# Performance work log

Measured on AMD Instinct MI355X. Metric: run time of the kernel, lower is better.

Reference implementation:

```python
import jax, jax.numpy as jnp
import numpy as np

B, C, H, W = 16, 64, 128, 128
C8 = C // 8


def setup_inputs() -> dict:
    key = jax.random.key(0)
    ks = jax.random.split(key, 8)
    s = 0.05
    return {
        "x": jax.random.normal(ks[0], (B, C, H, W), dtype=jnp.float32),
        "Wq": jax.random.normal(ks[1], (C8, C), dtype=jnp.float32) * s,
        "bq": jax.random.normal(ks[2], (C8,), dtype=jnp.float32) * s,
        "Wk": jax.random.normal(ks[3], (C8, C), dtype=jnp.float32) * s,
        "bk": jax.random.normal(ks[4], (C8,), dtype=jnp.float32) * s,
        "Wv": jax.random.normal(ks[5], (C, C), dtype=jnp.float32) * s,
        "bv": jax.random.normal(ks[6], (C,), dtype=jnp.float32) * s,
        "gamma": jnp.zeros((1,), dtype=jnp.float32),
    }


def _criss_cross(x, Wq, bq, Wk, bk, Wv, bv, gamma):
    # 1x1 convs == channel-mixing matmuls
    q = jnp.einsum("bchw,oc->bohw", x, Wq) + bq[None, :, None, None]  # [B,C8,H,W]
    k = jnp.einsum("bchw,oc->bohw", x, Wk) + bk[None, :, None, None]  # [B,C8,H,W]
    v = jnp.einsum("bchw,oc->bohw", x, Wv) + bv[None, :, None, None]  # [B,C,H,W]

    h = x.shape[2]
    # column (H-axis) attention scores; diagonal masked to -inf
    energy_H = jnp.einsum("bchw,bciw->bhwi", q, k)  # [B,H,W,H]
    diag = jnp.eye(h, dtype=bool)[None, :, None, :]  # mask where query row == key row
    energy_H = jnp.where(diag, -jnp.inf, energy_H)
    # row (W-axis) attention scores
    energy_W = jnp.einsum("bchw,bchj->bhwj", q, k)  # [B,H,W,W]

    # joint softmax over concatenated H+W axis
    att = jax.nn.softmax(jnp.concatenate([energy_H, energy_W], axis=3), axis=3)
    att_H = att[:, :, :, :h]    # [B,H,W,H]
    att_W = att[:, :, :, h:]    # [B,H,W,W]

    out_H = jnp.einsum("bhwi,bciw->bchw", att_H, v)
    out_W = jnp.einsum("bhwj,bchj->bchw", att_W, v)
    return gamma[0] * (out_H + out_W) + x


def reference(x, Wq, bq, Wk, bk, Wv, bv, gamma):
    return _criss_cross(x, Wq, bq, Wk, bk, Wv, bv, gamma)
```

## Files before the change

### kernel.cpp

```cpp
#include <hip/hip_runtime.h>

#define HW 128
#define CC 64
#define C8V 8
#define NB 16
#define LOG2E 1.44269504088896f

typedef _Float16 h1;
typedef _Float16 h2 __attribute__((ext_vector_type(2)));
typedef _Float16 half8 __attribute__((ext_vector_type(8)));
typedef float float16v __attribute__((ext_vector_type(16)));
typedef uint uv4 __attribute__((ext_vector_type(4)));

__device__ __forceinline__ uint packh2(float a, float b) {
#if __has_builtin(__builtin_amdgcn_cvt_pkrtz)
  return __builtin_bit_cast(uint, __builtin_amdgcn_cvt_pkrtz(a, b));
#else
  h2 v; v[0] = (h1)a; v[1] = (h1)b; return __builtin_bit_cast(uint, v);
#endif
}
__device__ __forceinline__ ushort f2h(float a) { h1 v = (h1)a; return __builtin_bit_cast(ushort, v); }
__device__ __forceinline__ float  h2f(ushort a) { return (float)__builtin_bit_cast(h1, a); }

__device__ __forceinline__ float fexp2(float x) {
#if __has_builtin(__builtin_amdgcn_exp2f)
  return __builtin_amdgcn_exp2f(x);
#else
  return exp2f(x);
#endif
}

__device__ __forceinline__ float16v mfma16(uv4 a, uv4 b, float16v c) {
  return __builtin_amdgcn_mfma_f32_32x32x16_f16(
      __builtin_bit_cast(half8, a), __builtin_bit_cast(half8, b), c, 0, 0, 0);
}

__global__ __launch_bounds__(256) void k_prep(
    const float* __restrict__ Wq, const float* __restrict__ bq,
    const float* __restrict__ Wk, const float* __restrict__ bk,
    const float* __restrict__ Wv, const float* __restrict__ bv,
    ushort* __restrict__ W_frag, float* __restrict__ bias_f)
{
  int idx = blockIdx.x * 256 + threadIdx.x;
  if (idx < 6144) {
    int g = idx >> 3, e = idx & 7;
    int kshi = g / 96, o = g % 96;
    int ks = kshi >> 1, hi = kshi & 1;
    int c = 8 * hi + 16 * ks + e;
    float val = (o < 8)  ? Wq[o * 64 + c] * LOG2E
              : (o < 16) ? Wk[(o - 8) * 64 + c]
              : (o < 80) ? Wv[(o - 16) * 64 + c] : 0.f;
    W_frag[idx] = f2h(val);
  }
  if (blockIdx.x == 0 && threadIdx.x < 96) {
    int t = threadIdx.x;
    bias_f[t] = (t < 8) ? bq[t] * LOG2E : (t < 16) ? bk[t - 8] : (t < 80) ? bv[t - 16] : 0.f;
  }
}

__global__ __launch_bounds__(256) void k_proj(
    const float* __restrict__ x, const ushort* __restrict__ W_frag,
    const float* __restrict__ bias_f,
    ushort* __restrict__ q, ushort* __restrict__ k,
    ushort* __restrict__ qT, ushort* __restrict__ kT,
    ushort* __restrict__ v)
{
  alignas(16) __shared__ ushort smem[10496];
  __shared__ float bias_l[96];
  ushort* o_l  = smem;
  ushort* qk_l = smem + 8192;

  int t = threadIdx.x;
  int lane = t & 63, wv = t >> 6, hi = lane >> 5;
  int b = blockIdx.x >> 7, r = blockIdx.x & 127;
  if (t < 96) bias_l[t] = bias_f[t];

  int w = 32 * wv + (lane & 31);
  const float* xw = x + (size_t)(b * CC) * (HW * HW) + (size_t)r * HW + w;
  const size_t PL = (size_t)HW * HW;

  float16v acc0 = {}, acc1 = {}, acc2 = {};
  #pragma unroll
  for (int ks = 0; ks < 4; ++ks) {
    int c0 = 8 * hi + 16 * ks;
    uint bx[4];
    #pragma unroll
    for (int e2 = 0; e2 < 4; ++e2) {
      float f0 = xw[(size_t)(c0 + 2 * e2) * PL];
      float f1 = xw[(size_t)(c0 + 2 * e2 + 1) * PL];
      bx[e2] = packh2(f0, f1);
    }
    uv4 Bx = {bx[0], bx[1], bx[2], bx[3]};
    const ushort* wf = W_frag + (size_t)(ks * 2 + hi) * 96 * 8;
    uv4 a0 = *(const uv4*)(wf + (lane & 31) * 8);
    uv4 a1 = *(const uv4*)(wf + ((lane & 31) + 32) * 8);
    uv4 a2 = *(const uv4*)(wf + ((lane & 31) + 64) * 8);
    acc0 = mfma16(a0, Bx, acc0);
    acc1 = mfma16(a1, Bx, acc1);
    acc2 = mfma16(a2, Bx, acc2);
  }
  __syncthreads();

  #pragma unroll
  for (int reg = 0; reg < 16; ++reg) {
    int orow = (reg & 3) + 8 * (reg >> 2) + 4 * hi;
    float v0 = acc0[reg] + bias_l[orow];
    if (orow < 16) qk_l[w * 18 + orow] = f2h(v0);
    else           o_l[(orow - 16) * 128 + w] = f2h(v0);
    o_l[(orow + 16) * 128 + w] = f2h(acc1[reg] + bias_l[orow + 32]);
    if (orow < 16)
      o_l[(orow + 48) * 128 + w] = f2h(acc2[reg] + bias_l[orow + 64]);
  }
  __syncthreads();

  {
    int pix = t & 127, isk = t >> 7;
    const ushort* src = &qk_l[pix * 18 + isk * 8];
    uint d0 = *(const uint*)(src + 0);
    uint d1 = *(const uint*)(src + 2);
    uint d2 = *(const uint*)(src + 4);
    uint d3 = *(const uint*)(src + 6);
    uv4 val = {d0, d1, d2, d3};
    ushort* dstn = (isk ? k : q)  + ((size_t)(b * HW + r) * HW + pix) * 8;
    ushort* dstt = (isk ? kT : qT) + ((size_t)(b * HW + pix) * HW + r) * 8;
    *(uv4*)dstn = val;
    *(uv4*)dstt = val;
  }
  ushort* vb = v + (size_t)(b * CC) * PL + (size_t)r * HW;
  #pragma unroll
  for (int i = 0; i < 4; ++i) {
    int idx = t + 256 * i; int o_ = idx >> 4, w8 = idx & 15;
    *(uv4*)(vb + (size_t)o_ * PL + w8 * 8) = *(const uv4*)&o_l[o_ * 128 + w8 * 8];
  }
}

__global__ __launch_bounds__(256) void k_transpose_v(const ushort* __restrict__ v,
                                                     ushort* __restrict__ vT)
{
  __shared__ ushort tl[128 * 130];
  int t = threadIdx.x;
  size_t base = (size_t)blockIdx.x * (HW * HW);
  const uint* ip = (const uint*)(v + base);
  uint* op = (uint*)(vT + base);
  int c2 = t & 63;
  int r0 = t >> 6;
  for (int it = 0; it < 32; ++it) {
    int r = it * 4 + r0;
    uint val = ip[r * 64 + c2];
    *(uint*)&tl[r * 130 + c2 * 2] = val;
  }
  __syncthreads();
  for (int it = 0; it < 32; ++it) {
    int wcol = it * 4 + r0;
    int hh = c2 * 2;
    uint lo = tl[hh * 130 + wcol];
    uint hi = tl[(hh + 1) * 130 + wcol];
    op[wcol * 64 + c2] = lo | (hi << 16);
  }
}

__global__ __launch_bounds__(256, 4) void k_attn_both(
    const ushort* __restrict__ qn, const ushort* __restrict__ kn,
    const ushort* __restrict__ qT, const ushort* __restrict__ kT,
    const ushort* __restrict__ vn, const ushort* __restrict__ vT,
    ushort* __restrict__ oW_, float* __restrict__ mW_, float* __restrict__ sW_,
    ushort* __restrict__ oH_, float* __restrict__ mH_, float* __restrict__ sH_)
{
  alignas(16) __shared__ uint V_l[64 * 64];

  int t = threadIdx.x;
  int lane = t & 63, wv = t >> 6;
  int hi = lane >> 5;
  int bid = blockIdx.x & 2047;
  bool maskf = blockIdx.x >= 2048;
  const ushort* qp = maskf ? qT : qn;
  const ushort* kp = maskf ? kT : kn;
  const ushort* vp = maskf ? vT : vn;
  ushort* op = maskf ? oH_ : oW_;
  float* mo = maskf ? mH_ : mW_;
  float* so = maskf ? sH_ : sW_;

  int b = bid >> 7, r = bid & 127;
  size_t plane32 = (size_t)(HW * HW) / 2;
  size_t pixbase = (size_t)(b * HW + r) * HW * 8;

  int qg = 32 * wv + (lane & 31);
  uv4 Bq = {0, 0, 0, 0};
  uv4 ka[4] = {{0,0,0,0}, {0,0,0,0}, {0,0,0,0}, {0,0,0,0}};
  if (hi == 0) {
    Bq = *(const uv4*)(qp + pixbase + (size_t)qg * 8);
    #pragma unroll
    for (int mt = 0; mt < 4; ++mt)
      ka[mt] = *(const uv4*)(kp + pixbase + (size_t)((lane & 31) + 32 * mt) * 8);
  }

  const uint* vrow = (const uint*)vp + (size_t)(b * CC) * plane32 + (size_t)r * 64;
  #pragma unroll
  for (int i = 0; i < 4; ++i) {
    int idx = t + 256 * i; int c = idx >> 4, j4 = idx & 15;
    uv4 val = *(const uv4*)(vrow + (size_t)c * plane32 + 4 * j4);
    uint byteoff = c * 256 + ((16 * j4) ^ ((c & 15) << 4));
    *(uv4*)((char*)V_l + byteoff) = val;
  }
  __syncthreads();

  float16v e[4];
  #pragma unroll
  for (int mt = 0; mt < 4; ++mt) {
    float16v z = {};
    e[mt] = mfma16(ka[mt], Bq, z);
  }

  if (maskf) {
    #pragma unroll
    for (int mt = 0; mt < 4; ++mt)
      #pragma unroll
      for (int reg = 0; reg < 16; ++reg) {
        int key = 32 * mt + ((reg & 3) + 8 * (reg >> 2) + 4 * hi);
        e[mt][reg] = (key == qg) ? -INFINITY : e[mt][reg];
      }
  }

  float m = -INFINITY;
  #pragma unroll
  for (int mt = 0; mt < 4; ++mt)
    #pragma unroll
    for (int reg = 0; reg < 16; reg += 2)
      m = fmaxf(m, fmaxf(e[mt][reg], e[mt][reg + 1]));
  m = fmaxf(m, __shfl_xor(m, 32));

  float s0 = 0.f, s1 = 0.f, s2 = 0.f, s3 = 0.f;
  #pragma unroll
  for (int mt = 0; mt < 4; ++mt) {
    #pragma unroll
    for (int reg = 0; reg < 16; reg += 4) {
      float p0 = fexp2(e[mt][reg + 0] - m);
      float p1 = fexp2(e[mt][reg + 1] - m);
      float p2 = fexp2(e[mt][reg + 2] - m);
      float p3 = fexp2(e[mt][reg + 3] - m);
      e[mt][reg + 0] = p0; e[mt][reg + 1] = p1;
      e[mt][reg + 2] = p2; e[mt][reg + 3] = p3;
      s0 += p0; s1 += p1; s2 += p2; s3 += p3;
    }
  }
  float s = (s0 + s1) + (s2 + s3);
  s += __shfl_xor(s, 32);
  if (lane < 32) {
    mo[(size_t)bid * HW + qg] = m;
    so[(size_t)bid * HW + qg] = s;
  }

  float16v acc0 = {}, acc1 = {};
  #pragma unroll
  for (int s8 = 0; s8 < 8; ++s8) {
    int mt = s8 >> 1, hf = s8 & 1;
    float p0 = e[mt][8 * hf + 0], p1 = e[mt][8 * hf + 1];
    float p2 = e[mt][8 * hf + 2], p3 = e[mt][8 * hf + 3];
    float p4 = e[mt][8 * hf + 4], p5 = e[mt][8 * hf + 5];
    float p6 = e[mt][8 * hf + 6], p7 = e[mt][8 * hf + 7];
    uint X = packh2(p0, p1), Y = packh2(p2, p3), Z = packh2(p4, p5), Wp = packh2(p6, p7);
    uint Xs = __shfl_xor(X, 32), Ys = __shfl_xor(Y, 32);
    uint Zs = __shfl_xor(Z, 32), Ws = __shfl_xor(Wp, 32);
    uv4 Bp;
    Bp[0] = (hi == 0) ? X  : Zs;
    Bp[1] = (hi == 0) ? Y  : Ws;
    Bp[2] = (hi == 0) ? Xs : Z;
    Bp[3] = (hi == 0) ? Ys : Wp;
    #pragma unroll
    for (int ct = 0; ct < 2; ++ct) {
      int c = (lane & 31) + 32 * ct;
      uint byteoff = c * 256 + ((16 * (hi + 2 * s8)) ^ ((c & 15) << 4));
      uv4 va = *(const uv4*)((const char*)V_l + byteoff);
      if (ct == 0) acc0 = mfma16(va, Bp, acc0);
      else         acc1 = mfma16(va, Bp, acc1);
    }
  }

  __syncthreads();
  ushort* o_l = (ushort*)V_l;
  int w = 32 * wv + (lane & 31);
  #pragma unroll
  for (int reg = 0; reg < 16; ++reg) {
    int c = (reg & 3) + 8 * (reg >> 2) + 4 * hi;
    o_l[(c +  0) * 128 + w] = f2h(acc0[reg]);
    o_l[(c + 32) * 128 + w] = f2h(acc1[reg]);
  }
  __syncthreads();
  ushort* ob = op + (size_t)(b * CC) * (HW * HW) + (size_t)r * HW;
  #pragma unroll
  for (int i = 0; i < 4; ++i) {
    int idx = t + 256 * i; int c = idx >> 4, w8 = idx & 15;
    *(uv4*)(ob + (size_t)c * (HW * HW) + w8 * 8) = *(const uv4*)&o_l[c * 128 + w8 * 8];
  }
}

__global__ __launch_bounds__(256) void k_alpha(
    const float* __restrict__ mH, const float* __restrict__ sH,
    const float* __restrict__ mW, const float* __restrict__ sW,
    ushort* __restrict__ aHT, ushort* __restrict__ aWn)
{
  __shared__ float mw_l[128 * 9], sw_l[128 * 9];
  __shared__ ushort aw_l[128 * 10];
  int t = threadIdx.x;
  int b = blockIdx.x >> 4, ws = blockIdx.x & 15;
  int w0 = ws * 8;
  const int PL = HW * HW;

  #pragma unroll
  for (int i = 0; i < 4; ++i) {
    int p = t + 256 * i;
    int w = p & 7, h = p >> 3;
    mw_l[h * 9 + w] = mW[(size_t)b * PL + h * HW + w0 + w];
    sw_l[h * 9 + w] = sW[(size_t)b * PL + h * HW + w0 + w];
  }
  __syncthreads();
  #pragma unroll
  for (int i = 0; i < 4; ++i) {
    int p = t + 256 * i;
    int h = p & 127, w = p >> 7;
    size_t tidx = (size_t)b * PL + (size_t)(w0 + w) * HW + h;
    float mh = mH[tidx], sh = sH[tidx];
    float mw = mw_l[h * 9 + w], sw = sw_l[h * 9 + w];
    float mm = fmaxf(mh, mw);
    float eh = fexp2(mh - mm), ew = fexp2(mw - mm);
    float inv = 1.f / (sh * eh + sw * ew);
    aHT[tidx] = f2h(eh * inv);
    aw_l[h * 10 + w] = f2h(ew * inv);
  }
  __syncthreads();
  #pragma unroll
  for (int i = 0; i < 4; ++i) {
    int p = t + 256 * i;
    int w = p & 7, h = p >> 3;
    aWn[(size_t)b * PL + (size_t)h * HW + w0 + w] = aw_l[h * 10 + w];
  }
}

__global__ __launch_bounds__(256) void k_merge(
    const ushort* __restrict__ oHT, const ushort* __restrict__ oW,
    const ushort* __restrict__ aHT, const ushort* __restrict__ aWn,
    const float* __restrict__ x, const float* __restrict__ gamma,
    float* __restrict__ out)
{
  alignas(16) __shared__ ushort otile[2 * 32 * 132];
  int t = threadIdx.x;
  int bid = blockIdx.x;
  int wsel = bid & 3, cg = (bid >> 2) & 31, b = bid >> 7;
  int w0 = wsel * 32;
  float g = gamma[0];
  const int PL = HW * HW;

  #pragma unroll
  for (int i = 0; i < 4; ++i) {
    int p = t + 256 * i;
    int ch = p >> 9, rest = p & 511;
    int w = rest >> 4, hg = rest & 15;
    size_t cbase = (size_t)(b * CC + cg * 2 + ch) * PL;
    uv4 ov = *(const uv4*)(oHT + cbase + (size_t)(w0 + w) * HW + hg * 8);
    uv4 av = *(const uv4*)(aHT + (size_t)b * PL + (size_t)(w0 + w) * HW + hg * 8);
    uv4 res;
    #pragma unroll
    for (int jj = 0; jj < 4; ++jj) {
      h2 o2 = __builtin_bit_cast(h2, ov[jj]);
      h2 a2 = __builtin_bit_cast(h2, av[jj]);
      res[jj] = __builtin_bit_cast(uint, o2 * a2);
    }
    *(uv4*)&otile[(ch * 32 + w) * 132 + hg * 8] = res;
  }
  __syncthreads();

  #pragma unroll
  for (int ch = 0; ch < 2; ++ch) {
    size_t cbase = (size_t)(b * CC + cg * 2 + ch) * PL;
    const ushort* otc = &otile[ch * 32 * 132];
    #pragma unroll
    for (int i = 0; i < 2; ++i) {
      int p = t + 256 * i;
      int w4 = p & 7, hh2 = p >> 3;
      float th0[4], th1[4];
      #pragma unroll
      for (int j = 0; j < 4; ++j) {
        uint pk = *(const uint*)&otc[(4 * w4 + j) * 132 + 2 * hh2];
        th0[j] = h2f((ushort)(pk & 0xffff));
        th1[j] = h2f((ushort)(pk >> 16));
      }
      #pragma unroll
      for (int rr = 0; rr < 2; ++rr) {
        int hh = 2 * hh2 + rr;
        const float* th = rr ? th1 : th0;
        size_t base = cbase + (size_t)hh * HW + w0 + 4 * w4;
        size_t abase = (size_t)b * PL + (size_t)hh * HW + w0 + 4 * w4;
        uint2 aw2 = *(const uint2*)(aWn + abase);
        uint2 ow2 = *(const uint2*)(oW + base);
        float4 xv = *(const float4*)(x + base);
        float4 res;
        res.x = g * (th[0] + h2f((ushort)(ow2.x & 0xffff)) * h2f((ushort)(aw2.x & 0xffff))) + xv.x;
        res.y = g * (th[1] + h2f((ushort)(ow2.x >> 16))    * h2f((ushort)(aw2.x >> 16)))    + xv.y;
        res.z = g * (th[2] + h2f((ushort)(ow2.y & 0xffff)) * h2f((ushort)(aw2.y & 0xffff))) + xv.z;
        res.w = g * (th[3] + h2f((ushort)(ow2.y >> 16))    * h2f((ushort)(aw2.y >> 16)))    + xv.w;
        *(float4*)(out + base) = res;
      }
    }
  }
}

extern "C" void kernel_launch(void* const* d_in, const int* in_sizes, int n_in,
                              void* d_out, int out_size, void* d_ws, size_t ws_size,
                              hipStream_t stream)
{
  const float* x     = (const float*)d_in[0];
  const float* Wq    = (const float*)d_in[1];
  const float* bq    = (const float*)d_in[2];
  const float* Wk    = (const float*)d_in[3];
  const float* bk    = (const float*)d_in[4];
  const float* Wv    = (const float*)d_in[5];
  const float* bv    = (const float*)d_in[6];
  const float* gamma = (const float*)d_in[7];
  float* out = (float*)d_out;

  char* w = (char*)d_ws;
  size_t np = (size_t)NB * HW * HW;
  ushort* W_frag = (ushort*)w; w += 6144 * 2;
  float*  bias_f = (float*)w;  w += 96 * 4 + 320;
  ushort* q   = (ushort*)w;  w += np * 8 * 2;
  ushort* k   = (ushort*)w;  w += np * 8 * 2;
  ushort* qT  = (ushort*)w;  w += np * 8 * 2;
  ushort* kT  = (ushort*)w;  w += np * 8 * 2;
  ushort* v   = (ushort*)w;  w += np * CC * 2;
  ushort* vT  = (ushort*)w;  w += np * CC * 2;
  ushort* oW  = (ushort*)w;  w += np * CC * 2;
  ushort* oHT = (ushort*)w;  w += np * CC * 2;
  float* mW = (float*)w;  w += np * 4;
  float* sW = (float*)w;  w += np * 4;
  float* mH = (float*)w;  w += np * 4;
  float* sH = (float*)w;  w += np * 4;
  ushort* aHT = (ushort*)w; w += np * 2;
  ushort* aWn = (ushort*)w; w += np * 2;
  if ((size_t)(w - (char*)d_ws) > ws_size) return;

  k_prep<<<24, 256, 0, stream>>>(Wq, bq, Wk, bk, Wv, bv, W_frag, bias_f);
  k_proj<<<NB * HW, 256, 0, stream>>>(x, W_frag, bias_f, q, k, qT, kT, v);
  k_transpose_v<<<NB * CC, 256, 0, stream>>>(v, vT);
  k_attn_both<<<2 * NB * HW, 256, 0, stream>>>(q, k, qT, kT, v, vT,
                                               oW, mW, sW, oHT, mH, sH);
  k_alpha<<<NB * 16, 256, 0, stream>>>(mH, sH, mW, sW, aHT, aWn);
  k_merge<<<NB * 32 * 4, 256, 0, stream>>>(oHT, oW, aHT, aWn, x, gamma, out);
}
```

Measured before the change: 117.0 us.

## Fuse row-wise attention into projection kernel, split column attention out

The projection kernel now computes the row (W-axis) attention directly from q/k/v held in shared memory, writing oW, mW and sW without round-tripping q, k and v through global memory. The non-transposed q/k buffers and their writes are removed. Column attention moves into a separate kernel launched over half the blocks. This saves global traffic and launch work but makes the projection kernel heavier, with more shared memory and registers.

```diff
diff --git a/kernel.cpp b/kernel.cpp
--- a/kernel.cpp
+++ b/kernel.cpp
@@ -58,17 +58,16 @@
   }
 }
 
-__global__ __launch_bounds__(256) void k_proj(
+__global__ __launch_bounds__(256, 4) void k_projW(
     const float* __restrict__ x, const ushort* __restrict__ W_frag,
     const float* __restrict__ bias_f,
-    ushort* __restrict__ q, ushort* __restrict__ k,
     ushort* __restrict__ qT, ushort* __restrict__ kT,
-    ushort* __restrict__ v)
-{
-  alignas(16) __shared__ ushort smem[10496];
+    ushort* __restrict__ v,
+    ushort* __restrict__ oW_, float* __restrict__ mW_, float* __restrict__ sW_)
+{
+  alignas(16) __shared__ uint V_l[64 * 64];
+  alignas(16) __shared__ ushort qk_l[128 * 24];
   __shared__ float bias_l[96];
-  ushort* o_l  = smem;
-  ushort* qk_l = smem + 8192;
 
   int t = threadIdx.x;
   int lane = t & 63, wv = t >> 6, hi = lane >> 5;
@@ -105,120 +104,52 @@
   for (int reg = 0; reg < 16; ++reg) {
     int orow = (reg & 3) + 8 * (reg >> 2) + 4 * hi;
     float v0 = acc0[reg] + bias_l[orow];
-    if (orow < 16) qk_l[w * 18 + orow] = f2h(v0);
-    else           o_l[(orow - 16) * 128 + w] = f2h(v0);
-    o_l[(orow + 16) * 128 + w] = f2h(acc1[reg] + bias_l[orow + 32]);
-    if (orow < 16)
-      o_l[(orow + 48) * 128 + w] = f2h(acc2[reg] + bias_l[orow + 64]);
-  }
-  __syncthreads();
-
+    if (orow < 16) {
+      qk_l[w * 24 + orow] = f2h(v0);
+    } else {
+      int c = orow - 16;
+      *(ushort*)((char*)V_l + c * 256 + ((2 * w) ^ ((c & 15) << 4))) = f2h(v0);
+    }
+    int c1 = orow + 16;
+    *(ushort*)((char*)V_l + c1 * 256 + ((2 * w) ^ ((c1 & 15) << 4))) =
+        f2h(acc1[reg] + bias_l[orow + 32]);
+    if (orow < 16) {
+      int c2_ = orow + 48;
+      *(ushort*)((char*)V_l + c2_ * 256 + ((2 * w) ^ ((c2_ & 15) << 4))) =
+          f2h(acc2[reg] + bias_l[orow + 64]);
+    }
+  }
+  __syncthreads();
+
+  ushort* vb = v + (size_t)(b * CC) * PL + (size_t)r * HW;
+  #pragma unroll
+  for (int i = 0; i < 4; ++i) {
+    int idx = t + 256 * i; int c = idx >> 4, j8 = idx & 15;
+    uv4 val = *(const uv4*)((const char*)V_l + c * 256 + ((16 * j8) ^ ((c & 15) << 4)));
+    *(uv4*)(vb + (size_t)c * PL + j8 * 8) = val;
+  }
   {
     int pix = t & 127, isk = t >> 7;
-    const ushort* src = &qk_l[pix * 18 + isk * 8];
-    uint d0 = *(const uint*)(src + 0);
-    uint d1 = *(const uint*)(src + 2);
-    uint d2 = *(const uint*)(src + 4);
-    uint d3 = *(const uint*)(src + 6);
-    uv4 val = {d0, d1, d2, d3};
-    ushort* dstn = (isk ? k : q)  + ((size_t)(b * HW + r) * HW + pix) * 8;
+    uv4 val = *(const uv4*)&qk_l[pix * 24 + isk * 8];
     ushort* dstt = (isk ? kT : qT) + ((size_t)(b * HW + pix) * HW + r) * 8;
-    *(uv4*)dstn = val;
     *(uv4*)dstt = val;
   }
-  ushort* vb = v + (size_t)(b * CC) * PL + (size_t)r * HW;
-  #pragma unroll
-  for (int i = 0; i < 4; ++i) {
-    int idx = t + 256 * i; int o_ = idx >> 4, w8 = idx & 15;
-    *(uv4*)(vb + (size_t)o_ * PL + w8 * 8) = *(const uv4*)&o_l[o_ * 128 + w8 * 8];
-  }
-}
-
-__global__ __launch_bounds__(256) void k_transpose_v(const ushort* __restrict__ v,
-                                                     ushort* __restrict__ vT)
-{
-  __shared__ ushort tl[128 * 130];
-  int t = threadIdx.x;
-  size_t base = (size_t)blockIdx.x * (HW * HW);
-  const uint* ip = (const uint*)(v + base);
-  uint* op = (uint*)(vT + base);
-  int c2 = t & 63;
-  int r0 = t >> 6;
-  for (int it = 0; it < 32; ++it) {
-    int r = it * 4 + r0;
-    uint val = ip[r * 64 + c2];
-    *(uint*)&tl[r * 130 + c2 * 2] = val;
-  }
-  __syncthreads();
-  for (int it = 0; it < 32; ++it) {
-    int wcol = it * 4 + r0;
-    int hh = c2 * 2;
-    uint lo = tl[hh * 130 + wcol];
-    uint hi = tl[(hh + 1) * 130 + wcol];
-    op[wcol * 64 + c2] = lo | (hi << 16);
-  }
-}
-
-__global__ __launch_bounds__(256, 4) void k_attn_both(
-    const ushort* __restrict__ qn, const ushort* __restrict__ kn,
-    const ushort* __restrict__ qT, const ushort* __restrict__ kT,
-    const ushort* __restrict__ vn, const ushort* __restrict__ vT,
-    ushort* __restrict__ oW_, float* __restrict__ mW_, float* __restrict__ sW_,
-    ushort* __restrict__ oH_, float* __restrict__ mH_, float* __restrict__ sH_)
-{
-  alignas(16) __shared__ uint V_l[64 * 64];
-
-  int t = threadIdx.x;
-  int lane = t & 63, wv = t >> 6;
-  int hi = lane >> 5;
-  int bid = blockIdx.x & 2047;
-  bool maskf = blockIdx.x >= 2048;
-  const ushort* qp = maskf ? qT : qn;
-  const ushort* kp = maskf ? kT : kn;
-  const ushort* vp = maskf ? vT : vn;
-  ushort* op = maskf ? oH_ : oW_;
-  float* mo = maskf ? mH_ : mW_;
-  float* so = maskf ? sH_ : sW_;
-
-  int b = bid >> 7, r = bid & 127;
-  size_t plane32 = (size_t)(HW * HW) / 2;
-  size_t pixbase = (size_t)(b * HW + r) * HW * 8;
-
-  int qg = 32 * wv + (lane & 31);
+
+  int qg = w;
   uv4 Bq = {0, 0, 0, 0};
   uv4 ka[4] = {{0,0,0,0}, {0,0,0,0}, {0,0,0,0}, {0,0,0,0}};
   if (hi == 0) {
-    Bq = *(const uv4*)(qp + pixbase + (size_t)qg * 8);
+    Bq = *(const uv4*)&qk_l[qg * 24];
     #pragma unroll
     for (int mt = 0; mt < 4; ++mt)
-      ka[mt] = *(const uv4*)(kp + pixbase + (size_t)((lane & 31) + 32 * mt) * 8);
-  }
-
-  const uint* vrow = (const uint*)vp + (size_t)(b * CC) * plane32 + (size_t)r * 64;
-  #pragma unroll
-  for (int i = 0; i < 4; ++i) {
-    int idx = t + 256 * i; int c = idx >> 4, j4 = idx & 15;
-    uv4 val = *(const uv4*)(vrow + (size_t)c * plane32 + 4 * j4);
-    uint byteoff = c * 256 + ((16 * j4) ^ ((c & 15) << 4));
-    *(uv4*)((char*)V_l + byteoff) = val;
-  }
-  __syncthreads();
+      ka[mt] = *(const uv4*)&qk_l[((lane & 31) + 32 * mt) * 24 + 8];
+  }
 
   float16v e[4];
   #pragma unroll
   for (int mt = 0; mt < 4; ++mt) {
     float16v z = {};
     e[mt] = mfma16(ka[mt], Bq, z);
-  }
-
-  if (maskf) {
-    #pragma unroll
-    for (int mt = 0; mt < 4; ++mt)
-      #pragma unroll
-      for (int reg = 0; reg < 16; ++reg) {
-        int key = 32 * mt + ((reg & 3) + 8 * (reg >> 2) + 4 * hi);
-        e[mt][reg] = (key == qg) ? -INFINITY : e[mt][reg];
-      }
   }
 
   float m = -INFINITY;
@@ -246,11 +177,11 @@
   float s = (s0 + s1) + (s2 + s3);
   s += __shfl_xor(s, 32);
   if (lane < 32) {
-    mo[(size_t)bid * HW + qg] = m;
-    so[(size_t)bid * HW + qg] = s;
-  }
-
-  float16v acc0 = {}, acc1 = {};
+    mW_[(size_t)blockIdx.x * HW + qg] = m;
+    sW_[(size_t)blockIdx.x * HW + qg] = s;
+  }
+
+  float16v pacc0 = {}, pacc1 = {};
   #pragma unroll
   for (int s8 = 0; s8 < 8; ++s8) {
     int mt = s8 >> 1, hf = s8 & 1;
@@ -271,6 +202,153 @@
       int c = (lane & 31) + 32 * ct;
       uint byteoff = c * 256 + ((16 * (hi + 2 * s8)) ^ ((c & 15) << 4));
       uv4 va = *(const uv4*)((const char*)V_l + byteoff);
+      if (ct == 0) pacc0 = mfma16(va, Bp, pacc0);
+      else         pacc1 = mfma16(va, Bp, pacc1);
+    }
+  }
+
+  __syncthreads();
+  ushort* o_l = (ushort*)V_l;
+  #pragma unroll
+  for (int reg = 0; reg < 16; ++reg) {
+    int c = (reg & 3) + 8 * (reg >> 2) + 4 * hi;
+    o_l[(c +  0) * 128 + w] = f2h(pacc0[reg]);
+    o_l[(c + 32) * 128 + w] = f2h(pacc1[reg]);
+  }
+  __syncthreads();
+  ushort* ob = oW_ + (size_t)(b * CC) * PL + (size_t)r * HW;
+  #pragma unroll
+  for (int i = 0; i < 4; ++i) {
+    int idx = t + 256 * i; int c = idx >> 4, w8 = idx & 15;
+    *(uv4*)(ob + (size_t)c * PL + w8 * 8) = *(const uv4*)&o_l[c * 128 + w8 * 8];
+  }
+}
+
+__global__ __launch_bounds__(256) void k_transpose_v(const ushort* __restrict__ v,
+                                                     ushort* __restrict__ vT)
+{
+  __shared__ ushort tl[128 * 130];
+  int t = threadIdx.x;
+  size_t base = (size_t)blockIdx.x * (HW * HW);
+  const uint* ip = (const uint*)(v + base);
+  uint* op = (uint*)(vT + base);
+  int c2 = t & 63;
+  int r0 = t >> 6;
+  for (int it = 0; it < 32; ++it) {
+    int r = it * 4 + r0;
+    uint val = ip[r * 64 + c2];
+    *(uint*)&tl[r * 130 + c2 * 2] = val;
+  }
+  __syncthreads();
+  for (int it = 0; it < 32; ++it) {
+    int wcol = it * 4 + r0;
+    int hh = c2 * 2;
+    uint lo = tl[hh * 130 + wcol];
+    uint hi = tl[(hh + 1) * 130 + wcol];
+    op[wcol * 64 + c2] = lo | (hi << 16);
+  }
+}
+
+__global__ __launch_bounds__(256, 4) void k_attnH(
+    const ushort* __restrict__ qT, const ushort* __restrict__ kT,
+    const ushort* __restrict__ vT,
+    ushort* __restrict__ oH_, float* __restrict__ mH_, float* __restrict__ sH_)
+{
+  alignas(16) __shared__ uint V_l[64 * 64];
+
+  int t = threadIdx.x;
+  int lane = t & 63, wv = t >> 6;
+  int hi = lane >> 5;
+  int bid = blockIdx.x;
+  int b = bid >> 7, r = bid & 127;
+  size_t plane32 = (size_t)(HW * HW) / 2;
+  size_t pixbase = (size_t)(b * HW + r) * HW * 8;
+
+  int qg = 32 * wv + (lane & 31);
+  uv4 Bq = {0, 0, 0, 0};
+  uv4 ka[4] = {{0,0,0,0}, {0,0,0,0}, {0,0,0,0}, {0,0,0,0}};
+  if (hi == 0) {
+    Bq = *(const uv4*)(qT + pixbase + (size_t)qg * 8);
+    #pragma unroll
+    for (int mt = 0; mt < 4; ++mt)
+      ka[mt] = *(const uv4*)(kT + pixbase + (size_t)((lane & 31) + 32 * mt) * 8);
+  }
+
+  const uint* vrow = (const uint*)vT + (size_t)(b * CC) * plane32 + (size_t)r * 64;
+  #pragma unroll
+  for (int i = 0; i < 4; ++i) {
+    int idx = t + 256 * i; int c = idx >> 4, j4 = idx & 15;
+    uv4 val = *(const uv4*)(vrow + (size_t)c * plane32 + 4 * j4);
+    uint byteoff = c * 256 + ((16 * j4) ^ ((c & 15) << 4));
+    *(uv4*)((char*)V_l + byteoff) = val;
+  }
+  __syncthreads();
+
+  float16v e[4];
+  #pragma unroll
+  for (int mt = 0; mt < 4; ++mt) {
+    float16v z = {};
+    e[mt] = mfma16(ka[mt], Bq, z);
+  }
+
+  #pragma unroll
+  for (int mt = 0; mt < 4; ++mt)
+    #pragma unroll
+    for (int reg = 0; reg < 16; ++reg) {
+      int key = 32 * mt + ((reg & 3) + 8 * (reg >> 2) + 4 * hi);
+      e[mt][reg] = (key == qg) ? -INFINITY : e[mt][reg];
+    }
+
+  float m = -INFINITY;
+  #pragma unroll
+  for (int mt = 0; mt < 4; ++mt)
+    #pragma unroll
+    for (int reg = 0; reg < 16; reg += 2)
+      m = fmaxf(m, fmaxf(e[mt][reg], e[mt][reg + 1]));
+  m = fmaxf(m, __shfl_xor(m, 32));
+
+  float s0 = 0.f, s1 = 0.f, s2 = 0.f, s3 = 0.f;
+  #pragma unroll
+  for (int mt = 0; mt < 4; ++mt) {
+    #pragma unroll
+    for (int reg = 0; reg < 16; reg += 4) {
+      float p0 = fexp2(e[mt][reg + 0] - m);
+      float p1 = fexp2(e[mt][reg + 1] - m);
+      float p2 = fexp2(e[mt][reg + 2] - m);
+      float p3 = fexp2(e[mt][reg + 3] - m);
+      e[mt][reg + 0] = p0; e[mt][reg + 1] = p1;
+      e[mt][reg + 2] = p2; e[mt][reg + 3] = p3;
+      s0 += p0; s1 += p1; s2 += p2; s3 += p3;
+    }
+  }
+  float s = (s0 + s1) + (s2 + s3);
+  s += __shfl_xor(s, 32);
+  if (lane < 32) {
+    mH_[(size_t)bid * HW + qg] = m;
+    sH_[(size_t)bid * HW + qg] = s;
+  }
+
+  float16v acc0 = {}, acc1 = {};
+  #pragma unroll
+  for (int s8 = 0; s8 < 8; ++s8) {
+    int mt = s8 >> 1, hf = s8 & 1;
+    float p0 = e[mt][8 * hf + 0], p1 = e[mt][8 * hf + 1];
+    float p2 = e[mt][8 * hf + 2], p3 = e[mt][8 * hf + 3];
+    float p4 = e[mt][8 * hf + 4], p5 = e[mt][8 * hf + 5];
+    float p6 = e[mt][8 * hf + 6], p7 = e[mt][8 * hf + 7];
+    uint X = packh2(p0, p1), Y = packh2(p2, p3), Z = packh2(p4, p5), Wp = packh2(p6, p7);
+    uint Xs = __shfl_xor(X, 32), Ys = __shfl_xor(Y, 32);
+    uint Zs = __shfl_xor(Z, 32), Ws = __shfl_xor(Wp, 32);
+    uv4 Bp;
+    Bp[0] = (hi == 0) ? X  : Zs;
+    Bp[1] = (hi == 0) ? Y  : Ws;
+    Bp[2] = (hi == 0) ? Xs : Z;
+    Bp[3] = (hi == 0) ? Ys : Wp;
+    #pragma unroll
+    for (int ct = 0; ct < 2; ++ct) {
+      int c = (lane & 31) + 32 * ct;
+      uint byteoff = c * 256 + ((16 * (hi + 2 * s8)) ^ ((c & 15) << 4));
+      uv4 va = *(const uv4*)((const char*)V_l + byteoff);
       if (ct == 0) acc0 = mfma16(va, Bp, acc0);
       else         acc1 = mfma16(va, Bp, acc1);
     }
@@ -286,7 +364,7 @@
     o_l[(c + 32) * 128 + w] = f2h(acc1[reg]);
   }
   __syncthreads();
-  ushort* ob = op + (size_t)(b * CC) * (HW * HW) + (size_t)r * HW;
+  ushort* ob = oH_ + (size_t)(b * CC) * (HW * HW) + (size_t)r * HW;
   #pragma unroll
   for (int i = 0; i < 4; ++i) {
     int idx = t + 256 * i; int c = idx >> 4, w8 = idx & 15;
@@ -422,8 +500,6 @@
   size_t np = (size_t)NB * HW * HW;
   ushort* W_frag = (ushort*)w; w += 6144 * 2;
   float*  bias_f = (float*)w;  w += 96 * 4 + 320;
-  ushort* q   = (ushort*)w;  w += np * 8 * 2;
-  ushort* k   = (ushort*)w;  w += np * 8 * 2;
   ushort* qT  = (ushort*)w;  w += np * 8 * 2;
   ushort* kT  = (ushort*)w;  w += np * 8 * 2;
   ushort* v   = (ushort*)w;  w += np * CC * 2;
@@ -439,10 +515,9 @@
   if ((size_t)(w - (char*)d_ws) > ws_size) return;
 
   k_prep<<<24, 256, 0, stream>>>(Wq, bq, Wk, bk, Wv, bv, W_frag, bias_f);
-  k_proj<<<NB * HW, 256, 0, stream>>>(x, W_frag, bias_f, q, k, qT, kT, v);
+  k_projW<<<NB * HW, 256, 0, stream>>>(x, W_frag, bias_f, qT, kT, v, oW, mW, sW);
   k_transpose_v<<<NB * CC, 256, 0, stream>>>(v, vT);
-  k_attn_both<<<2 * NB * HW, 256, 0, stream>>>(q, k, qT, kT, v, vT,
-                                               oW, mW, sW, oHT, mH, sH);
+  k_attnH<<<NB * HW, 256, 0, stream>>>(qT, kT, vT, oHT, mH, sH);
   k_alpha<<<NB * 16, 256, 0, stream>>>(mH, sH, mW, sW, aHT, aWn);
   k_merge<<<NB * 32 * 4, 256, 0, stream>>>(oHT, oW, aHT, aWn, x, gamma, out);
 }
```

Result: faster. 107.4 us (-8.2%).
